# Kernel tuning notes

Hardware: AMD Instinct MI355X
Metric: run time of the kernel (lower is better)

## Reference

```python
import jax, jax.numpy as jnp
import numpy as np

HEAD_DIM = 128


def block_causal_mask(cu_seqlens, seq_len, dtype):
    # positions -> which packed document each token belongs to
    positions = jnp.arange(seq_len)
    seq_ids = jnp.searchsorted(cu_seqlens, positions, side='right') - 1
    same_seq = seq_ids[:, None] == seq_ids[None, :]
    causal = positions[None, :] <= positions[:, None]  # key_pos <= query_pos
    neg_inf = jnp.asarray(float('-inf'), dtype)
    return jnp.where(same_seq & causal, jnp.asarray(0.0, dtype), neg_inf)


def setup_inputs() -> dict:
    key = jax.random.key(0)
    kq, kk, kv = jax.random.split(key, 3)
    B, H, S, D = 1, 8, 4096, HEAD_DIM
    q = jax.random.normal(kq, (B, H, S, D), dtype=jnp.float32)
    k = jax.random.normal(kk, (B, H, S, D), dtype=jnp.float32)
    v = jax.random.normal(kv, (B, H, S, D), dtype=jnp.float32)
    # 4 packed documents of length 1024 each; cu_seqlens[-1] == seq_len
    cu_seqlens = jnp.array([0, 1024, 2048, 3072, 4096], dtype=jnp.int32)
    return {"q": q, "k": k, "v": v, "cu_seqlens": cu_seqlens, "max_seqlen": 1024}


def reference(q, k, v, cu_seqlens, max_seqlen):
    seq_len = q.shape[2]
    scale = 1.0 / jnp.sqrt(jnp.asarray(q.shape[-1], q.dtype))
    mask = block_causal_mask(cu_seqlens, seq_len, q.dtype)  # [S, S]
    # scores: [B, H, Sq, Sk]
    scores = jnp.einsum('bhqd,bhkd->bhqk', q, k) * scale + mask
    probs = jax.nn.softmax(scores, axis=-1)
    return jnp.einsum('bhqk,bhkd->bhqd', probs, v)
```

## Files before the change

### kernel.cpp

```cpp
#include <hip/hip_runtime.h>
#include <hip/hip_bf16.h>


#define HD 128
#define BR 64
#define BC 64
#define KSTR 136
#define VSTR 33
#define PSTR 68

typedef __attribute__((ext_vector_type(8))) short short8;
typedef __attribute__((ext_vector_type(4))) short short4v;
typedef __attribute__((ext_vector_type(4))) float floatx4;

__device__ inline unsigned packbf2(float lo, float hi) {
    __hip_bfloat162 h2 = __float22bfloat162_rn(make_float2(lo, hi));
    return *reinterpret_cast<unsigned*>(&h2);
}
__device__ inline short bfs(float f) {
    __hip_bfloat16 b = __float2bfloat16(f);
    return *reinterpret_cast<short*>(&b);
}

union F4 { float4 v; float f[4]; };

__global__ __launch_bounds__(256, 2) void fa_fwd(
    const float* __restrict__ Q,
    const float* __restrict__ K,
    const float* __restrict__ V,
    const int* __restrict__ cu_seqlens, int n_cu,
    float* __restrict__ O,
    int S)
{
    __shared__ alignas(16) __hip_bfloat16 sK[2][BC * KSTR];
    __shared__ alignas(16) unsigned int   sVT[2][HD * VSTR];
    __shared__ alignas(16) __hip_bfloat16 sP[4][16 * PSTR];

    const int tid  = threadIdx.x;
    const int wave = tid >> 6;
    const int lane = tid & 63;
    const int quad = lane >> 4;
    const int l16  = lane & 15;

    const int dblk = tid & 31;
    const int trow = tid >> 5;
    const int vd    = tid & 127;
    const int vhalf = tid >> 7;

    const int nqb = S / BR;
    const int h   = blockIdx.x & 7;
    const int g   = (int)(blockIdx.x >> 3);
    int qb;
    if (nqb == 64) {
        if (g < 32) qb = (g >> 4) * 16 + (15 - (g & 15));
        else        qb = 32 + (((g - 32) >> 4) * 16) + (g & 15);
    } else {
        qb = nqb - 1 - g;
    }
    const int q0  = qb * BR;
    const int qw  = q0 + wave * 16;

    const size_t hoff = (size_t)h * S * HD;
    const float* Qh = Q + hoff;
    const float* Kh = K + hoff;
    const float* Vh = V + hoff;
    float*       Oh = O + hoff;

    int doc_start[4];
    #pragma unroll
    for (int r = 0; r < 4; ++r) {
        const int q = qw + quad * 4 + r;
        int dsr = 0;
        for (int i = 0; i < n_cu; ++i) {
            int c = cu_seqlens[i];
            if (c <= q) dsr = c;
        }
        doc_start[r] = dsr;
    }
    int blk_ds = 0;
    for (int i = 0; i < n_cu; ++i) {
        int c = cu_seqlens[i];
        if (c <= q0) blk_ds = c;
    }
    const int k_begin = blk_ds & ~(BC - 1);
    const int ntiles  = (q0 + BR - 1 - k_begin) / BC + 1;

    short8 aq[4];
    {
        const float* qp = Qh + (size_t)(qw + l16) * HD + quad * 8;
        #pragma unroll
        for (int ks = 0; ks < 4; ++ks) {
            float4 a0 = *(const float4*)(qp + ks * 32);
            float4 a1 = *(const float4*)(qp + ks * 32 + 4);
            short8 a;
            a[0] = bfs(a0.x); a[1] = bfs(a0.y); a[2] = bfs(a0.z); a[3] = bfs(a0.w);
            a[4] = bfs(a1.x); a[5] = bfs(a1.y); a[6] = bfs(a1.z); a[7] = bfs(a1.w);
            aq[ks] = a;
        }
    }

    floatx4 oacc[8];
    #pragma unroll
    for (int dt = 0; dt < 8; ++dt) oacc[dt] = (floatx4){0.f, 0.f, 0.f, 0.f};
    float m_r[4], l_r[4];
    #pragma unroll
    for (int r = 0; r < 4; ++r) { m_r[r] = -1e30f; l_r[r] = 0.f; }

    const float sl = 0.08838834764831845f * 1.4426950408889634f;

    F4 kf[8];
    float vf[32];

    auto issue_loads = [&](int kt) {
        const float* kb = Kh + (size_t)kt * HD + 4 * dblk;
        #pragma unroll
        for (int p = 0; p < 8; ++p)
            kf[p].v = *(const float4*)(kb + (size_t)(trow + 8 * p) * HD);
        const float* vb = Vh + (size_t)(kt + vhalf * 32) * HD + vd;
        #pragma unroll
        for (int kk = 0; kk < 32; ++kk)
            vf[kk] = vb[(size_t)kk * HD];
    };

    auto write_tiles = [&](int buf) {
        #pragma unroll
        for (int p = 0; p < 8; ++p) {
            uint2 kw;
            kw.x = packbf2(kf[p].f[0], kf[p].f[1]);
            kw.y = packbf2(kf[p].f[2], kf[p].f[3]);
            *(uint2*)(&sK[buf][(trow + 8 * p) * KSTR + 4 * dblk]) = kw;
        }
        unsigned* dst = &sVT[buf][vd * VSTR + vhalf * 16];
        #pragma unroll
        for (int kp = 0; kp < 16; ++kp)
            dst[kp] = packbf2(vf[2 * kp], vf[2 * kp + 1]);
    };

    issue_loads(k_begin);

    __hip_bfloat16* pbuf = &sP[wave][0];

    for (int it = 0; it < ntiles; ++it) {
        const int kt  = k_begin + it * BC;
        const int buf = it & 1;

        write_tiles(buf);
        __syncthreads();

        if (it + 1 < ntiles) issue_loads(kt + BC);

        floatx4 sc[4];
        #pragma unroll
        for (int ct = 0; ct < 4; ++ct) {
            if (kt + ct * 16 <= qw + 15) {
                floatx4 c = (floatx4){0.f, 0.f, 0.f, 0.f};
                #pragma unroll
                for (int ks = 0; ks < 4; ++ks) {
                    short8 b = *(const short8*)(&sK[buf][(ct * 16 + l16) * KSTR + ks * 32 + quad * 8]);
                    c = __builtin_amdgcn_mfma_f32_16x16x32_bf16(aq[ks], b, c, 0, 0, 0);
                }
                const int key = kt + ct * 16 + l16;
                #pragma unroll
                for (int r = 0; r < 4; ++r) {
                    const int q = qw + quad * 4 + r;
                    const bool valid = (key <= q) && (key >= doc_start[r]);
                    float s = c[r] * sl;
                    c[r] = valid ? s : -1e30f;
                }
                sc[ct] = c;
            } else {
                sc[ct] = (floatx4){-1e30f, -1e30f, -1e30f, -1e30f};
            }
        }

        float mx[4];
        #pragma unroll
        for (int r = 0; r < 4; ++r)
            mx[r] = fmaxf(fmaxf(sc[0][r], sc[1][r]), fmaxf(sc[2][r], sc[3][r]));
        #pragma unroll
        for (int off = 1; off < 16; off <<= 1) {
            #pragma unroll
            for (int r = 0; r < 4; ++r)
                mx[r] = fmaxf(mx[r], __shfl_xor(mx[r], off, 64));
        }
        float al[4];
        #pragma unroll
        for (int r = 0; r < 4; ++r) {
            const float mnew = fmaxf(m_r[r], mx[r]);
            al[r] = exp2f(m_r[r] - mnew);
            m_r[r] = mnew;
        }
        #pragma unroll
        for (int r = 0; r < 4; ++r) {
            float s0 = exp2f(sc[0][r] - m_r[r]);
            float s1 = exp2f(sc[1][r] - m_r[r]);
            float s2 = exp2f(sc[2][r] - m_r[r]);
            float s3 = exp2f(sc[3][r] - m_r[r]);
            sc[0][r] = s0; sc[1][r] = s1; sc[2][r] = s2; sc[3][r] = s3;
            l_r[r] = l_r[r] * al[r] + ((s0 + s1) + (s2 + s3));
        }
        #pragma unroll
        for (int dt = 0; dt < 8; ++dt) {
            #pragma unroll
            for (int r = 0; r < 4; ++r)
                oacc[dt][r] *= al[r];
        }

        #pragma unroll
        for (int ct = 0; ct < 4; ++ct)
            #pragma unroll
            for (int r = 0; r < 4; ++r)
                pbuf[(quad * 4 + r) * PSTR + ct * 16 + l16] = __float2bfloat16(sc[ct][r]);

        #pragma unroll
        for (int ks = 0; ks < 2; ++ks) {
            if (kt + ks * 32 <= qw + 15) {
                short4v lo = *(const short4v*)(&pbuf[l16 * PSTR + ks * 32 + quad * 8]);
                short4v hi = *(const short4v*)(&pbuf[l16 * PSTR + ks * 32 + quad * 8 + 4]);
                short8 ap = __builtin_shufflevector(lo, hi, 0, 1, 2, 3, 4, 5, 6, 7);
                #pragma unroll
                for (int dt = 0; dt < 8; ++dt) {
                    const unsigned* vp = &sVT[buf][(dt * 16 + l16) * VSTR + ks * 16 + quad * 4];
                    union { unsigned u[4]; short8 s; } cv;
                    cv.u[0] = vp[0]; cv.u[1] = vp[1]; cv.u[2] = vp[2]; cv.u[3] = vp[3];
                    oacc[dt] = __builtin_amdgcn_mfma_f32_16x16x32_bf16(ap, cv.s, oacc[dt], 0, 0, 0);
                }
            }
        }
    }

    #pragma unroll
    for (int off = 1; off < 16; off <<= 1) {
        #pragma unroll
        for (int r = 0; r < 4; ++r)
            l_r[r] += __shfl_xor(l_r[r], off, 64);
    }
    #pragma unroll
    for (int r = 0; r < 4; ++r) {
        const float inv = 1.0f / l_r[r];
        float* op = Oh + (size_t)(qw + quad * 4 + r) * HD;
        #pragma unroll
        for (int dt = 0; dt < 8; ++dt)
            op[dt * 16 + l16] = oacc[dt][r] * inv;
    }
}

extern "C" void kernel_launch(void* const* d_in, const int* in_sizes, int n_in,
                              void* d_out, int out_size, void* d_ws, size_t ws_size,
                              hipStream_t stream) {
    const float* q = (const float*)d_in[0];
    const float* k = (const float*)d_in[1];
    const float* v = (const float*)d_in[2];
    const int* cu = (const int*)d_in[3];
    const int n_cu = in_sizes[3];
    const int H = 8;
    const int S = in_sizes[0] / (H * HD);
    float* out = (float*)d_out;

    dim3 grid(H * (S / BR));
    dim3 block(256);
    fa_fwd<<<grid, block, 0, stream>>>(q, k, v, cu, n_cu, out, S);
}
```

Baseline: 131.3 us.

## Transpose MFMA operands so P stays in registers, drop LDS P round-trip

Swaps the A and B operands of both MFMAs so each lane owns one query row. The softmax row statistics then need only two cross-lane shuffles, and the bf16 P fragment can be packed directly from registers into the PV MFMA instead of going through a shared-memory P buffer. It also pads V^T to a 16-byte-aligned stride so V can be written and read with vector 128-bit LDS accesses, stores the output as float4, and raises wave priority around the MFMA sections. The intent is to remove the LDS traffic, barriers and shuffle overhead of the old layout; the padding change may alter LDS bank conflicts.

Result: no change. 128.9 us (-1.8%).

```diff
diff --git a/kernel.cpp b/kernel.cpp
--- a/kernel.cpp
+++ b/kernel.cpp
@@ -6,11 +6,9 @@
 #define BR 64
 #define BC 64
 #define KSTR 136
-#define VSTR 33
-#define PSTR 68
+#define VSTR 36
 
 typedef __attribute__((ext_vector_type(8))) short short8;
-typedef __attribute__((ext_vector_type(4))) short short4v;
 typedef __attribute__((ext_vector_type(4))) float floatx4;
 
 __device__ inline unsigned packbf2(float lo, float hi) {
@@ -34,7 +32,6 @@
 {
     __shared__ alignas(16) __hip_bfloat16 sK[2][BC * KSTR];
     __shared__ alignas(16) unsigned int   sVT[2][HD * VSTR];
-    __shared__ alignas(16) __hip_bfloat16 sP[4][16 * PSTR];
 
     const int tid  = threadIdx.x;
     const int wave = tid >> 6;
@@ -57,8 +54,9 @@
     } else {
         qb = nqb - 1 - g;
     }
-    const int q0  = qb * BR;
-    const int qw  = q0 + wave * 16;
+    const int q0    = qb * BR;
+    const int qw    = q0 + wave * 16;
+    const int qlane = qw + l16;
 
     const size_t hoff = (size_t)h * S * HD;
     const float* Qh = Q + hoff;
@@ -66,16 +64,10 @@
     const float* Vh = V + hoff;
     float*       Oh = O + hoff;
 
-    int doc_start[4];
-    #pragma unroll
-    for (int r = 0; r < 4; ++r) {
-        const int q = qw + quad * 4 + r;
-        int dsr = 0;
-        for (int i = 0; i < n_cu; ++i) {
-            int c = cu_seqlens[i];
-            if (c <= q) dsr = c;
-        }
-        doc_start[r] = dsr;
+    int ds_lane = 0;
+    for (int i = 0; i < n_cu; ++i) {
+        int c = cu_seqlens[i];
+        if (c <= qlane) ds_lane = c;
     }
     int blk_ds = 0;
     for (int i = 0; i < n_cu; ++i) {
@@ -87,7 +79,7 @@
 
     short8 aq[4];
     {
-        const float* qp = Qh + (size_t)(qw + l16) * HD + quad * 8;
+        const float* qp = Qh + (size_t)qlane * HD + quad * 8;
         #pragma unroll
         for (int ks = 0; ks < 4; ++ks) {
             float4 a0 = *(const float4*)(qp + ks * 32);
@@ -102,9 +94,7 @@
     floatx4 oacc[8];
     #pragma unroll
     for (int dt = 0; dt < 8; ++dt) oacc[dt] = (floatx4){0.f, 0.f, 0.f, 0.f};
-    float m_r[4], l_r[4];
-    #pragma unroll
-    for (int r = 0; r < 4; ++r) { m_r[r] = -1e30f; l_r[r] = 0.f; }
+    float m_r = -1e30f, l_r = 0.f;
 
     const float sl = 0.08838834764831845f * 1.4426950408889634f;
 
@@ -130,15 +120,19 @@
             kw.y = packbf2(kf[p].f[2], kf[p].f[3]);
             *(uint2*)(&sK[buf][(trow + 8 * p) * KSTR + 4 * dblk]) = kw;
         }
-        unsigned* dst = &sVT[buf][vd * VSTR + vhalf * 16];
-        #pragma unroll
-        for (int kp = 0; kp < 16; ++kp)
-            dst[kp] = packbf2(vf[2 * kp], vf[2 * kp + 1]);
+        unsigned* row = &sVT[buf][vd * VSTR + vhalf * 16];
+        #pragma unroll
+        for (int j = 0; j < 4; ++j) {
+            union { uint4 q; unsigned u[4]; } w;
+            w.u[0] = packbf2(vf[4*j],          vf[4*j + 1]);
+            w.u[1] = packbf2(vf[4*j + 2],      vf[4*j + 3]);
+            w.u[2] = packbf2(vf[16 + 4*j],     vf[16 + 4*j + 1]);
+            w.u[3] = packbf2(vf[16 + 4*j + 2], vf[16 + 4*j + 3]);
+            *(uint4*)(&row[4*j]) = w.q;
+        }
     };
 
     issue_loads(k_begin);
-
-    __hip_bfloat16* pbuf = &sP[wave][0];
 
     for (int it = 0; it < ntiles; ++it) {
         const int kt  = k_begin + it * BC;
@@ -150,98 +144,98 @@
         if (it + 1 < ntiles) issue_loads(kt + BC);
 
         floatx4 sc[4];
+        __builtin_amdgcn_s_setprio(1);
         #pragma unroll
         for (int ct = 0; ct < 4; ++ct) {
             if (kt + ct * 16 <= qw + 15) {
                 floatx4 c = (floatx4){0.f, 0.f, 0.f, 0.f};
                 #pragma unroll
                 for (int ks = 0; ks < 4; ++ks) {
-                    short8 b = *(const short8*)(&sK[buf][(ct * 16 + l16) * KSTR + ks * 32 + quad * 8]);
-                    c = __builtin_amdgcn_mfma_f32_16x16x32_bf16(aq[ks], b, c, 0, 0, 0);
-                }
-                const int key = kt + ct * 16 + l16;
-                #pragma unroll
-                for (int r = 0; r < 4; ++r) {
-                    const int q = qw + quad * 4 + r;
-                    const bool valid = (key <= q) && (key >= doc_start[r]);
-                    float s = c[r] * sl;
-                    c[r] = valid ? s : -1e30f;
+                    short8 a = *(const short8*)(&sK[buf][(ct * 16 + l16) * KSTR + ks * 32 + quad * 8]);
+                    c = __builtin_amdgcn_mfma_f32_16x16x32_bf16(a, aq[ks], c, 0, 0, 0);
                 }
                 sc[ct] = c;
             } else {
                 sc[ct] = (floatx4){-1e30f, -1e30f, -1e30f, -1e30f};
             }
         }
-
-        float mx[4];
-        #pragma unroll
-        for (int r = 0; r < 4; ++r)
-            mx[r] = fmaxf(fmaxf(sc[0][r], sc[1][r]), fmaxf(sc[2][r], sc[3][r]));
-        #pragma unroll
-        for (int off = 1; off < 16; off <<= 1) {
-            #pragma unroll
-            for (int r = 0; r < 4; ++r)
-                mx[r] = fmaxf(mx[r], __shfl_xor(mx[r], off, 64));
-        }
-        float al[4];
-        #pragma unroll
-        for (int r = 0; r < 4; ++r) {
-            const float mnew = fmaxf(m_r[r], mx[r]);
-            al[r] = exp2f(m_r[r] - mnew);
-            m_r[r] = mnew;
-        }
-        #pragma unroll
-        for (int r = 0; r < 4; ++r) {
-            float s0 = exp2f(sc[0][r] - m_r[r]);
-            float s1 = exp2f(sc[1][r] - m_r[r]);
-            float s2 = exp2f(sc[2][r] - m_r[r]);
-            float s3 = exp2f(sc[3][r] - m_r[r]);
-            sc[0][r] = s0; sc[1][r] = s1; sc[2][r] = s2; sc[3][r] = s3;
-            l_r[r] = l_r[r] * al[r] + ((s0 + s1) + (s2 + s3));
-        }
+        __builtin_amdgcn_s_setprio(0);
+
+        #pragma unroll
+        for (int ct = 0; ct < 4; ++ct) {
+            if (kt + ct * 16 <= qw + 15) {
+                #pragma unroll
+                for (int r = 0; r < 4; ++r) {
+                    const int key = kt + ct * 16 + quad * 4 + r;
+                    const bool valid = (key <= qlane) && (key >= ds_lane);
+                    float s = sc[ct][r] * sl;
+                    sc[ct][r] = valid ? s : -1e30f;
+                }
+            }
+        }
+
+        float mx0 = fmaxf(fmaxf(sc[0][0], sc[0][1]), fmaxf(sc[0][2], sc[0][3]));
+        float mx1 = fmaxf(fmaxf(sc[1][0], sc[1][1]), fmaxf(sc[1][2], sc[1][3]));
+        float mx2 = fmaxf(fmaxf(sc[2][0], sc[2][1]), fmaxf(sc[2][2], sc[2][3]));
+        float mx3 = fmaxf(fmaxf(sc[3][0], sc[3][1]), fmaxf(sc[3][2], sc[3][3]));
+        float mx  = fmaxf(fmaxf(mx0, mx1), fmaxf(mx2, mx3));
+        mx = fmaxf(mx, __shfl_xor(mx, 16, 64));
+        mx = fmaxf(mx, __shfl_xor(mx, 32, 64));
+
+        const float mnew = fmaxf(m_r, mx);
+        const float al   = exp2f(m_r - mnew);
+        m_r = mnew;
+
+        float s0 = 0.f, s1 = 0.f, s2 = 0.f, s3 = 0.f;
+        #pragma unroll
+        for (int ct = 0; ct < 4; ++ct) {
+            float p0 = exp2f(sc[ct][0] - m_r);
+            float p1 = exp2f(sc[ct][1] - m_r);
+            float p2 = exp2f(sc[ct][2] - m_r);
+            float p3 = exp2f(sc[ct][3] - m_r);
+            sc[ct][0] = p0; sc[ct][1] = p1; sc[ct][2] = p2; sc[ct][3] = p3;
+            s0 += p0; s1 += p1; s2 += p2; s3 += p3;
+        }
+        l_r = l_r * al + ((s0 + s1) + (s2 + s3));
         #pragma unroll
         for (int dt = 0; dt < 8; ++dt) {
             #pragma unroll
             for (int r = 0; r < 4; ++r)
-                oacc[dt][r] *= al[r];
-        }
-
-        #pragma unroll
-        for (int ct = 0; ct < 4; ++ct)
-            #pragma unroll
-            for (int r = 0; r < 4; ++r)
-                pbuf[(quad * 4 + r) * PSTR + ct * 16 + l16] = __float2bfloat16(sc[ct][r]);
-
+                oacc[dt][r] *= al;
+        }
+
+        __builtin_amdgcn_s_setprio(1);
         #pragma unroll
         for (int ks = 0; ks < 2; ++ks) {
             if (kt + ks * 32 <= qw + 15) {
-                short4v lo = *(const short4v*)(&pbuf[l16 * PSTR + ks * 32 + quad * 8]);
-                short4v hi = *(const short4v*)(&pbuf[l16 * PSTR + ks * 32 + quad * 8 + 4]);
-                short8 ap = __builtin_shufflevector(lo, hi, 0, 1, 2, 3, 4, 5, 6, 7);
+                union { unsigned u[4]; short8 s; } pu;
+                pu.u[0] = packbf2(sc[2*ks][0],   sc[2*ks][1]);
+                pu.u[1] = packbf2(sc[2*ks][2],   sc[2*ks][3]);
+                pu.u[2] = packbf2(sc[2*ks+1][0], sc[2*ks+1][1]);
+                pu.u[3] = packbf2(sc[2*ks+1][2], sc[2*ks+1][3]);
                 #pragma unroll
                 for (int dt = 0; dt < 8; ++dt) {
-                    const unsigned* vp = &sVT[buf][(dt * 16 + l16) * VSTR + ks * 16 + quad * 4];
-                    union { unsigned u[4]; short8 s; } cv;
-                    cv.u[0] = vp[0]; cv.u[1] = vp[1]; cv.u[2] = vp[2]; cv.u[3] = vp[3];
-                    oacc[dt] = __builtin_amdgcn_mfma_f32_16x16x32_bf16(ap, cv.s, oacc[dt], 0, 0, 0);
+                    union { uint4 q; short8 s; } cv;
+                    cv.q = *(const uint4*)(&sVT[buf][(dt * 16 + l16) * VSTR + ks * 16 + quad * 4]);
+                    oacc[dt] = __builtin_amdgcn_mfma_f32_16x16x32_bf16(cv.s, pu.s, oacc[dt], 0, 0, 0);
                 }
             }
         }
-    }
-
+        __builtin_amdgcn_s_setprio(0);
+    }
+
+    l_r += __shfl_xor(l_r, 16, 64);
+    l_r += __shfl_xor(l_r, 32, 64);
+    const float inv = 1.0f / l_r;
+    float* op = Oh + (size_t)qlane * HD + quad * 4;
     #pragma unroll
-    for (int off = 1; off < 16; off <<= 1) {
-        #pragma unroll
-        for (int r = 0; r < 4; ++r)
-            l_r[r] += __shfl_xor(l_r[r], off, 64);
-    }
-    #pragma unroll
-    for (int r = 0; r < 4; ++r) {
-        const float inv = 1.0f / l_r[r];
-        float* op = Oh + (size_t)(qw + quad * 4 + r) * HD;
-        #pragma unroll
-        for (int dt = 0; dt < 8; ++dt)
-            op[dt * 16 + l16] = oacc[dt][r] * inv;
+    for (int dt = 0; dt < 8; ++dt) {
+        float4 st;
+        st.x = oacc[dt][0] * inv;
+        st.y = oacc[dt][1] * inv;
+        st.z = oacc[dt][2] * inv;
+        st.w = oacc[dt][3] * inv;
+        *(float4*)(op + dt * 16) = st;
     }
 }
 
```
